# Kernel optimization log

Hardware: AMD Instinct MI355X
Metric: run time of the kernel (lower is better)

The kernel has to match this reference:

```python
import jax, jax.numpy as jnp
import numpy as np

NEG_BIG = -9e15  # matches torch's -9000000000000000.0 mask value
ALPHA = 0.2      # LeakyReLU negative slope


def setup_inputs() -> dict:
    key = jax.random.key(0)
    k1, k2, k3 = jax.random.split(key, 3)
    B, N, Fin, Fout = 8, 2048, 64, 64
    h = jax.random.normal(k1, (B, N, Fin), dtype=jnp.float32)
    adj = jax.random.randint(k2, (B, N, N), 0, 2, dtype=jnp.int32)
    kW, ka = jax.random.split(k3)
    # xavier_uniform with gain=1.414
    gW = 1.414 * np.sqrt(6.0 / (Fin + Fout))
    W = jax.random.uniform(kW, (Fin, Fout), minval=-gW, maxval=gW, dtype=jnp.float32)
    ga = 1.414 * np.sqrt(6.0 / (2 * Fout + 1))
    a = jax.random.uniform(ka, (2 * Fout, 1), minval=-ga, maxval=ga, dtype=jnp.float32)
    return {"h": h, "adj": adj, "W": W, "a": a}


def reference(h, adj, W, a):
    # Wh: [B, N, Fout]
    Wh = jnp.einsum("bnf,fo->bno", h, W)
    Fout = W.shape[1]
    a1 = a[:Fout, 0]   # source part of attention vector
    a2 = a[Fout:, 0]   # target part
    # e_ij = leakyrelu(a1.Wh_i + a2.Wh_j) -- rank-1 decomposition of the
    # repeat/cat construction; avoids the [B,N,N,2F] intermediate.
    s = Wh @ a1        # [B, N]
    t = Wh @ a2        # [B, N]
    e = s[:, :, None] + t[:, None, :]            # [B, N, N]
    e = jnp.where(e > 0, e, ALPHA * e)           # LeakyReLU
    e = jnp.where(adj > 0, e, NEG_BIG)           # adjacency mask
    attention = jax.nn.softmax(e, axis=2)
    # dropout omitted: reference is eval-mode (F.dropout is identity when not training)
    h_prime = jnp.einsum("bij,bjo->bio", attention, Wh)
    return jax.nn.elu(h_prime)                   # concat=True branch
```

## Files before the change

kernel.cpp:

```cpp
#include <hip/hip_runtime.h>


#define ALPHA 0.2f

typedef __attribute__((ext_vector_type(8))) short  short8;
typedef __attribute__((ext_vector_type(4))) float  f32x4;

static __device__ __forceinline__ unsigned short f2bf(float f) {
    unsigned u = __builtin_bit_cast(unsigned, f);
    u += 0x7fffu + ((u >> 16) & 1u);
    return (unsigned short)(u >> 16);
}

static __device__ __forceinline__ unsigned pack_bf2(float lo, float hi) {
    unsigned ulo = __builtin_bit_cast(unsigned, lo) + 0x8000u;
    unsigned uhi = __builtin_bit_cast(unsigned, hi) + 0x8000u;
    return __builtin_amdgcn_perm(uhi, ulo, 0x07060302);
}

__global__ __launch_bounds__(256) void k1_wh_st(
    const float* __restrict__ h, const float* __restrict__ W,
    const float* __restrict__ a, uint4* __restrict__ whF,
    float* __restrict__ sw, float* __restrict__ tw)
{
    __shared__ float W_l[64 * 65];
    __shared__ float wa[128];
    __shared__ float tile[4 * 16 * 65];

    const int tid  = threadIdx.x;
    const int lane = tid & 63, wv = tid >> 6;
    const int im   = lane & 15, kq = lane >> 4;

    #pragma unroll
    for (int k = 0; k < 16; ++k) {
        int e = tid + 256 * k;
        W_l[(e >> 6) * 65 + (e & 63)] = W[e];
    }
    __syncthreads();

    if (tid < 128) {
        int f = tid & 63;
        const float* ap = a + (tid >> 6) * 64;
        float acc = 0.f;
        #pragma unroll 8
        for (int o = 0; o < 64; ++o) acc += W_l[f * 65 + o] * ap[o];
        wa[tid] = acc;
    }
    __syncthreads();

    short8 bf[4][2];
    #pragma unroll
    for (int nb = 0; nb < 4; ++nb)
        #pragma unroll
        for (int ks = 0; ks < 2; ++ks)
            #pragma unroll
            for (int u = 0; u < 8; ++u)
                bf[nb][ks][u] = (short)f2bf(W_l[(ks * 32 + kq * 8 + u) * 65 + nb * 16 + im]);

    const int row0 = blockIdx.x * 64 + wv * 16;
    const float* hrow = h + (size_t)(row0 + im) * 64;

    float hv[2][8];
    short8 af[2];
    float sp = 0.f, tp = 0.f;
    #pragma unroll
    for (int ks = 0; ks < 2; ++ks) {
        float4 A = *(const float4*)(hrow + ks * 32 + kq * 8);
        float4 Bv = *(const float4*)(hrow + ks * 32 + kq * 8 + 4);
        hv[ks][0] = A.x;  hv[ks][1] = A.y;  hv[ks][2] = A.z;  hv[ks][3] = A.w;
        hv[ks][4] = Bv.x; hv[ks][5] = Bv.y; hv[ks][6] = Bv.z; hv[ks][7] = Bv.w;
        #pragma unroll
        for (int u = 0; u < 8; ++u) {
            int f = ks * 32 + kq * 8 + u;
            sp += hv[ks][u] * wa[f];
            tp += hv[ks][u] * wa[64 + f];
            af[ks][u] = (short)f2bf(hv[ks][u]);
        }
    }
    sp += __shfl_xor(sp, 16, 64); sp += __shfl_xor(sp, 32, 64);
    tp += __shfl_xor(tp, 16, 64); tp += __shfl_xor(tp, 32, 64);
    if (lane < 16) {
        sw[row0 + lane] = sp;
        tw[row0 + lane] = tp;
    }

    f32x4 acc[4] = {{0.f,0.f,0.f,0.f},{0.f,0.f,0.f,0.f},{0.f,0.f,0.f,0.f},{0.f,0.f,0.f,0.f}};
    #pragma unroll
    for (int ks = 0; ks < 2; ++ks)
        #pragma unroll
        for (int nb = 0; nb < 4; ++nb)
            acc[nb] = __builtin_amdgcn_mfma_f32_16x16x32_bf16(af[ks], bf[nb][ks], acc[nb], 0, 0, 0);

    #pragma unroll
    for (int nb = 0; nb < 4; ++nb)
        #pragma unroll
        for (int r = 0; r < 4; ++r)
            tile[wv * 1040 + (kq * 4 + r) * 65 + nb * 16 + im] = acc[nb][r];
    __syncthreads();

    {
        const int blk_row0 = blockIdx.x * 64;
        const int bb2 = blk_row0 >> 11;
        const int c_base = (blk_row0 & 2047) >> 5;
        #pragma unroll
        for (int k = 0; k < 2; ++k) {
            int e = tid + 256 * k;
            int l = e & 63, ot = (e >> 6) & 3, cl_ = e >> 8;
            int o = ot * 16 + (l & 15);
            int jb = cl_ * 32 + (l >> 4) * 8;
            unsigned d0, d1, d2, d3;
            {
                int j0 = jb;
                d0 = pack_bf2(tile[(j0 >> 4) * 1040 + (j0 & 15) * 65 + o],
                              tile[(j0 >> 4) * 1040 + ((j0 & 15) + 1) * 65 + o]);
                j0 = jb + 2;
                d1 = pack_bf2(tile[(j0 >> 4) * 1040 + (j0 & 15) * 65 + o],
                              tile[(j0 >> 4) * 1040 + ((j0 & 15) + 1) * 65 + o]);
                j0 = jb + 4;
                d2 = pack_bf2(tile[(j0 >> 4) * 1040 + (j0 & 15) * 65 + o],
                              tile[(j0 >> 4) * 1040 + ((j0 & 15) + 1) * 65 + o]);
                j0 = jb + 6;
                d3 = pack_bf2(tile[(j0 >> 4) * 1040 + (j0 & 15) * 65 + o],
                              tile[(j0 >> 4) * 1040 + ((j0 & 15) + 1) * 65 + o]);
            }
            uint4 val = {d0, d1, d2, d3};
            whF[(size_t)(((bb2 * 64 + c_base + cl_) * 4 + ot)) * 64 + l] = val;
        }
    }
}

__global__ __launch_bounds__(256, 4) void k2_attn(
    const int* __restrict__ adj, const uint4* __restrict__ whF,
    const float* __restrict__ sw, const float* __restrict__ tw,
    float* __restrict__ out)
{
    __shared__ float eB[2048];
    __shared__ float eD[2048];
    __shared__ unsigned blt[128 * 4 * 2];
    __shared__ float cpart[4 * 1040];
    __shared__ float zp[64];

    const int tid  = threadIdx.x;
    const int lane = tid & 63, wv = tid >> 6;
    const int im   = lane & 15, kq = lane >> 4;
    const int b    = blockIdx.x >> 7;
    const int i0   = (blockIdx.x & 127) << 4;

    {
        const int4* a4 = (const int4*)(adj + (size_t)(b * 2048 + i0) * 2048);
        #pragma unroll 4
        for (int k = 0; k < 32; ++k) {
            const int chunk = k * 4 + wv;
            const int4 v = a4[(chunk >> 3) * 512 + (chunk & 7) * 64 + lane];
            unsigned long long B0 = __ballot(v.x != 0);
            unsigned long long B1 = __ballot(v.y != 0);
            unsigned long long B2 = __ballot(v.z != 0);
            unsigned long long B3 = __ballot(v.w != 0);
            if (lane < 4) {
                unsigned long long bv = lane == 0 ? B0 : lane == 1 ? B1 : lane == 2 ? B2 : B3;
                *(unsigned long long*)&blt[(chunk * 4 + lane) * 2] = bv;
            }
        }
    }

    {
        const float4* tp4 = (const float4*)(tw + (size_t)b * 2048);
        float4 t0 = tp4[tid], t1 = tp4[tid + 256];
        float4 e0 = {__expf(t0.x), __expf(t0.y), __expf(t0.z), __expf(t0.w)};
        float4 e1 = {__expf(t1.x), __expf(t1.y), __expf(t1.z), __expf(t1.w)};
        float4 f0 = {__expf(ALPHA*t0.x), __expf(ALPHA*t0.y), __expf(ALPHA*t0.z), __expf(ALPHA*t0.w)};
        float4 f1 = {__expf(ALPHA*t1.x), __expf(ALPHA*t1.y), __expf(ALPHA*t1.z), __expf(ALPHA*t1.w)};
        *(float4*)&eB[tid * 4] = e0;  *(float4*)&eB[(tid + 256) * 4] = e1;
        *(float4*)&eD[tid * 4] = f0;  *(float4*)&eD[(tid + 256) * 4] = f1;
    }

    const float sl = sw[b * 2048 + i0 + im];
    const float al = __expf(sl), cl_ = __expf(ALPHA * sl);
    const int j00 = wv * 512 + kq * 8;
    const uint4* wbase = whF + (size_t)((b * 64 + wv * 16) * 4) * 64 + lane;

    short8 ones;
    #pragma unroll
    for (int u = 0; u < 8; ++u) ones[u] = (short)0x3F80;

    __syncthreads();

    unsigned mpk[4] = {0u, 0u, 0u, 0u};
    #pragma unroll
    for (int s = 0; s < 16; ++s) {
        const int chunk = im * 8 + wv * 2 + (s >> 3);
        const int l0 = ((s & 7) << 3) + 2 * kq;
        const int wsel = l0 >> 5, p = l0 & 31;
        unsigned byte = 0;
        #pragma unroll
        for (int c = 0; c < 4; ++c) {
            unsigned two = (blt[(chunk * 4 + c) * 2 + wsel] >> p) & 3u;
            byte |= (two & 1u) << c;
            byte |= (two >> 1) << (4 + c);
        }
        mpk[s >> 2] |= byte << ((s & 3) * 8);
    }

    f32x4 acc0 = {0.f,0.f,0.f,0.f}, acc1 = {0.f,0.f,0.f,0.f};
    f32x4 acc2 = {0.f,0.f,0.f,0.f}, acc3 = {0.f,0.f,0.f,0.f};
    f32x4 accz = {0.f,0.f,0.f,0.f};

    uint4 c0 = wbase[0], c1 = wbase[64], c2 = wbase[128], c3 = wbase[192];

    #pragma unroll
    for (int s = 0; s < 16; ++s) {
        uint4 n0, n1, n2, n3;
        if (s < 15) {
            n0 = wbase[(s + 1) * 256      ];
            n1 = wbase[(s + 1) * 256 +  64];
            n2 = wbase[(s + 1) * 256 + 128];
            n3 = wbase[(s + 1) * 256 + 192];
        } else {
            n0 = c0; n1 = c1; n2 = c2; n3 = c3;
        }

        const float4 bA  = *(const float4*)&eB[j00 + s * 32];
        const float4 bBv = *(const float4*)&eB[j00 + s * 32 + 4];
        const float4 dA  = *(const float4*)&eD[j00 + s * 32];
        const float4 dBv = *(const float4*)&eD[j00 + s * 32 + 4];
        const unsigned mbyte = (mpk[s >> 2] >> ((s & 3) * 8)) & 0xffu;

        float p0 = fmaxf(al * bA.x,  cl_ * dA.x);   p0 = (mbyte &   1u) ? p0 : 0.f;
        float p1 = fmaxf(al * bA.y,  cl_ * dA.y);   p1 = (mbyte &   2u) ? p1 : 0.f;
        float p2 = fmaxf(al * bA.z,  cl_ * dA.z);   p2 = (mbyte &   4u) ? p2 : 0.f;
        float p3 = fmaxf(al * bA.w,  cl_ * dA.w);   p3 = (mbyte &   8u) ? p3 : 0.f;
        float p4 = fmaxf(al * bBv.x, cl_ * dBv.x);  p4 = (mbyte &  16u) ? p4 : 0.f;
        float p5 = fmaxf(al * bBv.y, cl_ * dBv.y);  p5 = (mbyte &  32u) ? p5 : 0.f;
        float p6 = fmaxf(al * bBv.z, cl_ * dBv.z);  p6 = (mbyte &  64u) ? p6 : 0.f;
        float p7 = fmaxf(al * bBv.w, cl_ * dBv.w);  p7 = (mbyte & 128u) ? p7 : 0.f;

        int4 ai;
        ai.x = (int)pack_bf2(p0, p1);
        ai.y = (int)pack_bf2(p2, p3);
        ai.z = (int)pack_bf2(p4, p5);
        ai.w = (int)pack_bf2(p6, p7);
        const short8 af = __builtin_bit_cast(short8, ai);

        acc0 = __builtin_amdgcn_mfma_f32_16x16x32_bf16(af, __builtin_bit_cast(short8, c0), acc0, 0, 0, 0);
        acc1 = __builtin_amdgcn_mfma_f32_16x16x32_bf16(af, __builtin_bit_cast(short8, c1), acc1, 0, 0, 0);
        acc2 = __builtin_amdgcn_mfma_f32_16x16x32_bf16(af, __builtin_bit_cast(short8, c2), acc2, 0, 0, 0);
        acc3 = __builtin_amdgcn_mfma_f32_16x16x32_bf16(af, __builtin_bit_cast(short8, c3), acc3, 0, 0, 0);
        accz = __builtin_amdgcn_mfma_f32_16x16x32_bf16(af, ones, accz, 0, 0, 0);

        c0 = n0; c1 = n1; c2 = n2; c3 = n3;
    }

    if (im == 0) {
        #pragma unroll
        for (int r = 0; r < 4; ++r) zp[wv * 16 + kq * 4 + r] = accz[r];
    }

    #pragma unroll
    for (int r = 0; r < 4; ++r) {
        cpart[wv * 1040 + (kq * 4 + r) * 65 +  0 + im] = acc0[r];
        cpart[wv * 1040 + (kq * 4 + r) * 65 + 16 + im] = acc1[r];
        cpart[wv * 1040 + (kq * 4 + r) * 65 + 32 + im] = acc2[r];
        cpart[wv * 1040 + (kq * 4 + r) * 65 + 48 + im] = acc3[r];
    }
    __syncthreads();

    #pragma unroll
    for (int k = 0; k < 4; ++k) {
        int idx = tid + 256 * k;
        int i = idx >> 6, o = idx & 63;
        float ssum = cpart[0 * 1040 + i * 65 + o] + cpart[1 * 1040 + i * 65 + o]
                   + cpart[2 * 1040 + i * 65 + o] + cpart[3 * 1040 + i * 65 + o];
        float z = zp[i] + zp[16 + i] + zp[32 + i] + zp[48 + i];
        if (z == 0.f) z = 1.f;
        float r = ssum / z;
        out[((size_t)(b * 2048 + i0 + i)) * 64 + o] = r > 0.f ? r : expm1f(r);
    }
}

extern "C" void kernel_launch(void* const* d_in, const int* in_sizes, int n_in,
                              void* d_out, int out_size, void* d_ws, size_t ws_size,
                              hipStream_t stream) {
    const float* h   = (const float*)d_in[0];
    const int*   adj = (const int*)d_in[1];
    const float* W   = (const float*)d_in[2];
    const float* a   = (const float*)d_in[3];
    float* out = (float*)d_out;

    uint4* whF = (uint4*)d_ws;
    float* sw  = (float*)((char*)d_ws + 2097152);
    float* tw  = (float*)((char*)d_ws + 2097152 + 65536);

    hipLaunchKernelGGL(k1_wh_st, dim3(256), dim3(256), 0, stream, h, W, a, whF, sw, tw);
    hipLaunchKernelGGL(k2_attn, dim3(1024), dim3(256), 0, stream, adj, whF, sw, tw, out);
}
```

Before: 215.7 us.

## Split adjacency bit-packing into a separate kernel feeding the attention kernel

Moves the ballot-based packing of the int32 adjacency matrix into bitmasks out of the attention kernel and into a dedicated ka_pack kernel that writes packed bits to workspace. The attention kernel then loads its packed mask rows straight from global memory and no longer needs the shared-memory mask table. This frees LDS and shortens the attention kernel's prologue, which may raise occupancy. The cost is an extra launch and a global round trip for the packed mask, while the dominant 128 MB adjacency read stays.

```diff
diff --git a/kernel.cpp b/kernel.cpp
--- a/kernel.cpp
+++ b/kernel.cpp
@@ -16,6 +16,43 @@
     unsigned ulo = __builtin_bit_cast(unsigned, lo) + 0x8000u;
     unsigned uhi = __builtin_bit_cast(unsigned, hi) + 0x8000u;
     return __builtin_amdgcn_perm(uhi, ulo, 0x07060302);
+}
+
+__global__ __launch_bounds__(256) void ka_pack(
+    const int* __restrict__ adj, unsigned* __restrict__ blt)
+{
+    const int tid  = threadIdx.x;
+    const int lane = tid & 63, wv = tid >> 6;
+    const size_t Wd = (size_t)blockIdx.x * 4 + wv;
+    const int4* a4 = (const int4*)adj;
+    const size_t base = Wd * 1024 + lane;
+
+    #pragma unroll
+    for (int hh = 0; hh < 2; ++hh) {
+        int4 v0 = a4[base + (hh * 8 + 0) * 64];
+        int4 v1 = a4[base + (hh * 8 + 1) * 64];
+        int4 v2 = a4[base + (hh * 8 + 2) * 64];
+        int4 v3 = a4[base + (hh * 8 + 3) * 64];
+        int4 v4 = a4[base + (hh * 8 + 4) * 64];
+        int4 v5 = a4[base + (hh * 8 + 5) * 64];
+        int4 v6 = a4[base + (hh * 8 + 6) * 64];
+        int4 v7 = a4[base + (hh * 8 + 7) * 64];
+        #pragma unroll
+        for (int q = 0; q < 8; ++q) {
+            int4 v = q == 0 ? v0 : q == 1 ? v1 : q == 2 ? v2 : q == 3 ? v3
+                   : q == 4 ? v4 : q == 5 ? v5 : q == 6 ? v6 : v7;
+            unsigned long long B0 = __ballot(v.x != 0);
+            unsigned long long B1 = __ballot(v.y != 0);
+            unsigned long long B2 = __ballot(v.z != 0);
+            unsigned long long B3 = __ballot(v.w != 0);
+            if (lane < 8) {
+                const int c = lane >> 1, half = lane & 1;
+                unsigned long long Bc = c == 0 ? B0 : c == 1 ? B1 : c == 2 ? B2 : B3;
+                unsigned val = (unsigned)(Bc >> (32 * half));
+                blt[(Wd * 16 + hh * 8 + q) * 8 + lane] = val;
+            }
+        }
+    }
 }
 
 __global__ __launch_bounds__(256) void k1_wh_st(
@@ -130,13 +167,12 @@
 }
 
 __global__ __launch_bounds__(256, 4) void k2_attn(
-    const int* __restrict__ adj, const uint4* __restrict__ whF,
+    const unsigned* __restrict__ blt, const uint4* __restrict__ whF,
     const float* __restrict__ sw, const float* __restrict__ tw,
     float* __restrict__ out)
 {
     __shared__ float eB[2048];
     __shared__ float eD[2048];
-    __shared__ unsigned blt[128 * 4 * 2];
     __shared__ float cpart[4 * 1040];
     __shared__ float zp[64];
 
@@ -146,22 +182,9 @@
     const int b    = blockIdx.x >> 7;
     const int i0   = (blockIdx.x & 127) << 4;
 
-    {
-        const int4* a4 = (const int4*)(adj + (size_t)(b * 2048 + i0) * 2048);
-        #pragma unroll 4
-        for (int k = 0; k < 32; ++k) {
-            const int chunk = k * 4 + wv;
-            const int4 v = a4[(chunk >> 3) * 512 + (chunk & 7) * 64 + lane];
-            unsigned long long B0 = __ballot(v.x != 0);
-            unsigned long long B1 = __ballot(v.y != 0);
-            unsigned long long B2 = __ballot(v.z != 0);
-            unsigned long long B3 = __ballot(v.w != 0);
-            if (lane < 4) {
-                unsigned long long bv = lane == 0 ? B0 : lane == 1 ? B1 : lane == 2 ? B2 : B3;
-                *(unsigned long long*)&blt[(chunk * 4 + lane) * 2] = bv;
-            }
-        }
-    }
+    const uint4* bp = (const uint4*)(blt
+                    + ((size_t)(b * 2048 + i0 + im) * 8 + 2 * wv) * 8);
+    const uint4 q0 = bp[0], q1 = bp[1], q2 = bp[2], q3 = bp[3];
 
     {
         const float4* tp4 = (const float4*)(tw + (size_t)b * 2048);
@@ -174,6 +197,26 @@
         *(float4*)&eD[tid * 4] = f0;  *(float4*)&eD[(tid + 256) * 4] = f1;
     }
 
+    unsigned mpk[4] = {0u, 0u, 0u, 0u};
+    #pragma unroll
+    for (int s = 0; s < 16; ++s) {
+        const int half = (s & 7) >> 2;
+        unsigned w0, w1, w2, w3;
+        if (s < 8) {
+            w0 = half ? q0.y : q0.x;  w1 = half ? q0.w : q0.z;
+            w2 = half ? q1.y : q1.x;  w3 = half ? q1.w : q1.z;
+        } else {
+            w0 = half ? q2.y : q2.x;  w1 = half ? q2.w : q2.z;
+            w2 = half ? q3.y : q3.x;  w3 = half ? q3.w : q3.z;
+        }
+        const int p = 8 * ((s & 7) & 3) + 2 * kq;
+        unsigned t0 = (w0 >> p) & 3u, t1 = (w1 >> p) & 3u;
+        unsigned t2 = (w2 >> p) & 3u, t3 = (w3 >> p) & 3u;
+        unsigned byte = (t0 & 1u) | ((t1 & 1u) << 1) | ((t2 & 1u) << 2) | ((t3 & 1u) << 3)
+                      | ((t0 >> 1) << 4) | ((t1 >> 1) << 5) | ((t2 >> 1) << 6) | ((t3 >> 1) << 7);
+        mpk[s >> 2] |= byte << ((s & 3) * 8);
+    }
+
     const float sl = sw[b * 2048 + i0 + im];
     const float al = __expf(sl), cl_ = __expf(ALPHA * sl);
     const int j00 = wv * 512 + kq * 8;
@@ -184,22 +227,6 @@
     for (int u = 0; u < 8; ++u) ones[u] = (short)0x3F80;
 
     __syncthreads();
-
-    unsigned mpk[4] = {0u, 0u, 0u, 0u};
-    #pragma unroll
-    for (int s = 0; s < 16; ++s) {
-        const int chunk = im * 8 + wv * 2 + (s >> 3);
-        const int l0 = ((s & 7) << 3) + 2 * kq;
-        const int wsel = l0 >> 5, p = l0 & 31;
-        unsigned byte = 0;
-        #pragma unroll
-        for (int c = 0; c < 4; ++c) {
-            unsigned two = (blt[(chunk * 4 + c) * 2 + wsel] >> p) & 3u;
-            byte |= (two & 1u) << c;
-            byte |= (two >> 1) << (4 + c);
-        }
-        mpk[s >> 2] |= byte << ((s & 3) * 8);
-    }
 
     f32x4 acc0 = {0.f,0.f,0.f,0.f}, acc1 = {0.f,0.f,0.f,0.f};
     f32x4 acc2 = {0.f,0.f,0.f,0.f}, acc3 = {0.f,0.f,0.f,0.f};
@@ -289,7 +316,9 @@
     uint4* whF = (uint4*)d_ws;
     float* sw  = (float*)((char*)d_ws + 2097152);
     float* tw  = (float*)((char*)d_ws + 2097152 + 65536);
+    unsigned* blt = (unsigned*)((char*)d_ws + 2097152 + 131072);
 
     hipLaunchKernelGGL(k1_wh_st, dim3(256), dim3(256), 0, stream, h, W, a, whF, sw, tw);
-    hipLaunchKernelGGL(k2_attn, dim3(1024), dim3(256), 0, stream, adj, whF, sw, tw, out);
-}
+    hipLaunchKernelGGL(ka_pack, dim3(2048), dim3(256), 0, stream, adj, blt);
+    hipLaunchKernelGGL(k2_attn, dim3(1024), dim3(256), 0, stream, blt, whF, sw, tw, out);
+}
```

Measured after the change: 222.8 us. +3.3%, slower.
